# Performance work log

Hardware: AMD Instinct MI355X
Metric: run time of the kernel (lower is better)

The kernel has to match this reference:

```python
import jax, jax.numpy as jnp
import numpy as np

N_HEAD = 16
N_EMBD = 1024
HEAD_DIM = N_EMBD // N_HEAD  # 64
ROPE_BASE = 10000.0


def _rotary_cos_sin(T, dim, dtype=jnp.float32):
    # matches Rotary: inv_freq over even indices, cos/sin cached in bfloat16
    inv_freq = 1.0 / (ROPE_BASE ** (jnp.arange(0, dim, 2, dtype=jnp.float32) / dim))
    freqs = jnp.arange(T, dtype=jnp.float32)[:, None] * inv_freq[None, :]  # [T, dim/2]
    cos = jnp.cos(freqs).astype(jnp.bfloat16).astype(dtype)
    sin = jnp.sin(freqs).astype(jnp.bfloat16).astype(dtype)
    # shape [1, T, 1, dim/2] to broadcast over (B, T, H, d)
    return cos[None, :, None, :], sin[None, :, None, :]


def _apply_rotary(x, cos, sin):
    d = x.shape[3] // 2
    x1, x2 = x[..., :d], x[..., d:]
    y1 = x1 * cos + x2 * sin
    y2 = -x1 * sin + x2 * cos
    return jnp.concatenate([y1, y2], axis=3).astype(x.dtype)


def setup_inputs() -> dict:
    key = jax.random.key(0)
    ks = jax.random.split(key, 8)
    B, T, C = 2, 2048, N_EMBD
    scale = C ** -0.5  # realistic linear-layer init scale
    x = jax.random.normal(ks[0], (B, T, C), dtype=jnp.float32)
    Wq1 = jax.random.normal(ks[1], (C, C), dtype=jnp.float32) * scale
    Wk1 = jax.random.normal(ks[2], (C, C), dtype=jnp.float32) * scale
    Wq2 = jax.random.normal(ks[3], (C, C), dtype=jnp.float32) * scale
    Wk2 = jax.random.normal(ks[4], (C, C), dtype=jnp.float32) * scale
    Wv = jax.random.normal(ks[5], (C, C), dtype=jnp.float32) * scale
    Wout = jax.random.normal(ks[6], (C, C), dtype=jnp.float32) * scale
    return {"x": x, "Wq1": Wq1, "Wk1": Wk1, "Wq2": Wq2, "Wk2": Wk2, "Wv": Wv, "Wout": Wout}


def reference(x, Wq1, Wk1, Wq2, Wk2, Wv, Wout):
    B, T, C = x.shape
    H, D = N_HEAD, HEAD_DIM

    def proj(W):
        # torch nn.Linear(bias=False): y = x @ W.T
        return (x @ W.T).reshape(B, T, H, D)

    q1, k1 = proj(Wq1), proj(Wk1)
    q2, k2 = proj(Wq2), proj(Wk2)
    v = proj(Wv)

    cos, sin = _rotary_cos_sin(T, D, x.dtype)
    q1, k1 = _apply_rotary(q1, cos, sin), _apply_rotary(k1, cos, sin)
    q2, k2 = _apply_rotary(q2, cos, sin), _apply_rotary(k2, cos, sin)

    # two bilinear score maps, elementwise product, causal mask
    s1 = jnp.einsum('bqhd,bkhd->bhqk', q1, k1)  # [B,H,T,T]
    s2 = jnp.einsum('bqhd,bkhd->bhqk', q2, k2)
    causal = jnp.tril(jnp.ones((T, T), dtype=bool))
    pattern = jnp.where(causal[None, None], (s1 / D) * (s2 / D), 0.0)

    y = jnp.einsum('bhqk,bkhd->bqhd', pattern, v).reshape(B, T, C)
    return y @ Wout.T
```

## Files before the change

### kernel.cpp

```cpp
#include <hip/hip_runtime.h>
#include <hip/hip_bf16.h>
#include <math.h>

typedef __bf16 bf16;
typedef __bf16 bf16x8 __attribute__((ext_vector_type(8)));
typedef float  f32x4  __attribute__((ext_vector_type(4)));

#define NB    2
#define NT    2048
#define NH    16
#define ND    64
#define NC    1024
#define NBT   4096
#define NQT   32

#define AS1C(p) ((const __attribute__((address_space(1))) void*)(p))
#define AS3(p)  ((__attribute__((address_space(3))) void*)(p))

#define MFMA(a,b,c) __builtin_amdgcn_mfma_f32_16x16x32_bf16(a, b, c, 0, 0, 0)

__global__ void cast_kernel(const float* __restrict__ src, bf16* __restrict__ dst, int n)
{
    int i = (blockIdx.x * blockDim.x + threadIdx.x) * 4;
    if (i + 3 < n) {
        float4 v = *reinterpret_cast<const float4*>(src + i);
        dst[i+0] = (bf16)v.x;
        dst[i+1] = (bf16)v.y;
        dst[i+2] = (bf16)v.z;
        dst[i+3] = (bf16)v.w;
    }
}

struct WPtrs { const float* p[6]; };
__global__ void cast6_kernel(WPtrs w, bf16* __restrict__ dst)
{
    const int mat = blockIdx.x >> 10;
    const int off = ((blockIdx.x & 1023) * 256 + threadIdx.x) * 4;
    float4 v = *reinterpret_cast<const float4*>(w.p[mat] + off);
    bf16* d = dst + (size_t)mat * NC * NC + off;
    d[0] = (bf16)v.x; d[1] = (bf16)v.y; d[2] = (bf16)v.z; d[3] = (bf16)v.w;
}

__global__ void rope_table_kernel(float2* __restrict__ tbl)
{
    int i = blockIdx.x * 256 + threadIdx.x;
    int t = i >> 5, j = i & 31;
    float invf = 1.0f / powf(10000.0f, (float)j * (1.0f/32.0f));
    float fr = (float)t * invf;
    float2 cs;
    cs.x = (float)(bf16)cosf(fr);
    cs.y = (float)(bf16)sinf(fr);
    tbl[i] = cs;
}

__global__ __launch_bounds__(512, 1)
void gemm_proj(const bf16* __restrict__ A, const bf16* __restrict__ Bw,
               bf16* __restrict__ qkv, const float2* __restrict__ tbl)
{
    __shared__ bf16 smem[2*32768];

    const int tid  = threadIdx.x;
    const int lane = tid & 63;
    const int w    = tid >> 6;
    const int wr   = w >> 2;
    const int wc   = w & 3;

    const int id  = blockIdx.x;
    const int swz = (id & 7) * 40 + (id >> 3);
    const int by  = swz / 20, bx = swz % 20;
    const int row0 = by * 256, col0 = bx * 256;

    const int lo  = lane & 15;
    const int hi  = lane >> 4;

    const int srow = tid >> 3;
    const int ssw  = ((tid & 7) ^ (srow & 7)) * 8;

    f32x4 acc[8][4] = {};

    auto stage = [&](int buf, int kt) {
        char* As = (char*)smem + buf*65536;
        char* Bs = As + 32768;
        #pragma unroll
        for (int i = 0; i < 4; ++i) {
            const unsigned loff = (unsigned)(i*8192 + w*1024);
            __builtin_amdgcn_global_load_lds(
                AS1C(A + (size_t)(row0 + i*64 + srow) * NC + kt + ssw),
                AS3(As + loff), 16, 0, 0);
            __builtin_amdgcn_global_load_lds(
                AS1C(Bw + (size_t)(col0 + i*64 + srow) * NC + kt + ssw),
                AS3(Bs + loff), 16, 0, 0);
        }
    };

    stage(0, 0);
    asm volatile("s_waitcnt vmcnt(0)" ::: "memory");
    __syncthreads();

    for (int kt = 0; kt < 16; ++kt) {
        const int cur = kt & 1;
        if (kt < 15) stage(cur ^ 1, (kt + 1) * 64);

        const char* As = (const char*)smem + cur*65536;
        const char* Bs = As + 32768;

        __builtin_amdgcn_s_setprio(1);
        #pragma unroll
        for (int ks = 0; ks < 2; ++ks) {
            bf16x8 af[8], bfr[4];
            #pragma unroll
            for (int m = 0; m < 8; ++m) {
                const int ar = wr*128 + m*16 + lo;
                af[m] = *reinterpret_cast<const bf16x8*>(
                    As + ar*128 + (((ks*4 + hi) ^ (lo & 7)) * 16));
            }
            #pragma unroll
            for (int n = 0; n < 4; ++n) {
                const int br = wc*64 + n*16 + lo;
                bfr[n] = *reinterpret_cast<const bf16x8*>(
                    Bs + br*128 + (((ks*4 + hi) ^ (lo & 7)) * 16));
            }
            #pragma unroll
            for (int m = 0; m < 8; ++m)
                #pragma unroll
                for (int n = 0; n < 4; ++n)
                    acc[m][n] = MFMA(af[m], bfr[n], acc[m][n]);
        }
        __builtin_amdgcn_s_setprio(0);

        asm volatile("s_waitcnt vmcnt(0)" ::: "memory");
        __syncthreads();
    }

    bf16* Ct = smem;
    const int p  = col0 >> 10;
    const int h0 = (col0 >> 6) & (NH-1);
    const int rb = hi * 4;

    if (p < 4) {
        const float qsc = (p == 0 || p == 2) ? 0.015625f : 1.0f;
        #pragma unroll
        for (int m = 0; m < 8; ++m)
            #pragma unroll
            for (int r = 0; r < 4; ++r) {
                const int rl = wr*128 + m*16 + rb + r;
                const int t  = (row0 + rl) & (NT-1);
                const unsigned key = ((unsigned)(rl >> 2) & 3) << 5;
                #pragma unroll
                for (int n = 0; n < 2; ++n) {
                    const int j = n*16 + lo;
                    float2 cs = tbl[t*32 + j];
                    float a1 = acc[m][n][r];
                    float a2 = acc[m][n+2][r];
                    const int c1 = wc*64 + j;
                    const int c2 = c1 + 32;
                    *(bf16*)((char*)Ct + (unsigned)(rl*512 + (((unsigned)c1*2) ^ key)))
                        = (bf16)((a1*cs.x + a2*cs.y) * qsc);
                    *(bf16*)((char*)Ct + (unsigned)(rl*512 + (((unsigned)c2*2) ^ key)))
                        = (bf16)((a2*cs.x - a1*cs.y) * qsc);
                }
            }
        __syncthreads();
        #pragma unroll
        for (int it = 0; it < 16; ++it) {
            const int chunk = it*512 + tid;
            const int rl = chunk >> 5;
            const int cc = chunk & 31;
            const unsigned key = ((unsigned)(rl >> 2) & 3) << 5;
            bf16x8 val = *reinterpret_cast<const bf16x8*>(
                (const char*)Ct + (unsigned)(rl*512 + (((unsigned)cc*16) ^ key)));
            const int rowg = row0 + rl;
            const int b = rowg >> 11;
            const int t = rowg & (NT-1);
            const int hh = h0 + (cc >> 3);
            const int d  = (cc & 7) * 8;
            *reinterpret_cast<bf16x8*>(
                qkv + ((((size_t)p*NB + b)*NH + hh)*NT + t)*ND + d) = val;
        }
    } else {
        #pragma unroll
        for (int m = 0; m < 8; ++m)
            #pragma unroll
            for (int r = 0; r < 4; ++r) {
                const int rl = wr*128 + m*16 + rb + r;
                #pragma unroll
                for (int n = 0; n < 4; ++n) {
                    const int c = wc*64 + n*16 + lo;
                    *(bf16*)((char*)Ct + (unsigned)(c*512 + (((unsigned)rl*2) ^ ((c&7)<<4))))
                        = (bf16)acc[m][n][r];
                }
            }
        __syncthreads();
        const int b  = row0 >> 11;
        const int t0 = row0 & (NT-1);
        #pragma unroll
        for (int it = 0; it < 16; ++it) {
            const int chunk = it*512 + tid;
            const int c   = chunk >> 5;
            const int tcc = chunk & 31;
            bf16x8 val = *reinterpret_cast<const bf16x8*>(
                (const char*)Ct + (unsigned)(c*512 + (((unsigned)tcc*16) ^ ((c&7)<<4))));
            const int hh = h0 + (c >> 6);
            const int d  = c & 63;
            *reinterpret_cast<bf16x8*>(
                qkv + (((size_t)4*NB + b)*NH + hh)*(size_t)NT*ND
                    + (size_t)d*NT + t0 + tcc*8) = val;
        }
    }
}

__global__ __launch_bounds__(256)
void gemm_out(const bf16* __restrict__ A, const bf16* __restrict__ Bw,
              float* __restrict__ Cp, int M, int N, int K)
{
    __shared__ bf16 smem[128*128];
    bf16* As = smem;
    bf16* Bs = smem + 128*64;

    const int tid  = threadIdx.x;
    const int lane = tid & 63;
    const int w    = tid >> 6;
    const int wr   = w >> 1;
    const int wc   = w & 1;
    const int row0 = blockIdx.y * 128;
    const int col0 = blockIdx.x * 128;

    const int lo   = lane & 15;
    const int hi8  = (lane >> 4) * 8;
    const int srow = w * 8 + (lane >> 3);
    const int scol = (lane & 7) * 8;

    f32x4 acc[4][4] = {};

    for (int kt = 0; kt < K; kt += 64) {
        #pragma unroll
        for (int i = 0; i < 4; ++i) {
            const unsigned loff = (unsigned)(i * 4096 + w * 1024);
            __builtin_amdgcn_global_load_lds(
                AS1C(A + (size_t)(row0 + i*32 + srow) * K + kt + scol),
                AS3((char*)As + loff), 16, 0, 0);
            __builtin_amdgcn_global_load_lds(
                AS1C(Bw + (size_t)(col0 + i*32 + srow) * K + kt + scol),
                AS3((char*)Bs + loff), 16, 0, 0);
        }
        __syncthreads();
        #pragma unroll
        for (int ks = 0; ks < 2; ++ks) {
            bf16x8 af[4], bfr[4];
            #pragma unroll
            for (int m = 0; m < 4; ++m)
                af[m] = *reinterpret_cast<const bf16x8*>(&As[(wr*64 + m*16 + lo)*64 + ks*32 + hi8]);
            #pragma unroll
            for (int n = 0; n < 4; ++n)
                bfr[n] = *reinterpret_cast<const bf16x8*>(&Bs[(wc*64 + n*16 + lo)*64 + ks*32 + hi8]);
            #pragma unroll
            for (int m = 0; m < 4; ++m)
                #pragma unroll
                for (int n = 0; n < 4; ++n)
                    acc[m][n] = MFMA(af[m], bfr[n], acc[m][n]);
        }
        __syncthreads();
    }

    const int rb = (lane >> 4) * 4;
    #pragma unroll
    for (int m = 0; m < 4; ++m)
        #pragma unroll
        for (int n = 0; n < 4; ++n)
            #pragma unroll
            for (int r = 0; r < 4; ++r) {
                int row = row0 + wr*64 + m*16 + rb + r;
                int col = col0 + wc*64 + n*16 + lo;
                Cp[(size_t)row * N + col] = acc[m][n][r];
            }
}

__global__ __launch_bounds__(256, 2)
void attn_kernel(const bf16* __restrict__ qkv, bf16* __restrict__ Y)
{
    __shared__ bf16 K1s[2*4096];
    __shared__ bf16 K2s[2*4096];
    __shared__ bf16 Vts[2*4096];
    __shared__ bf16 Pa [4][1024];
    __shared__ bf16 Pb [4][1024];

    const int tid  = threadIdx.x;
    const int lane = tid & 63;
    const int w    = tid >> 6;

    const int lin  = blockIdx.x;
    const int xcd  = lin & 7;
    const int slot = lin >> 3;
    const int pair = xcd * 4 + (slot >> 4);
    const int qa   = slot & 15;
    const int h    = pair >> 1;
    const int b    = pair & 1;
    const int qb   = NQT - 1 - qa;

    const size_t plane = (size_t)NB * NH * NT * ND;
    const size_t bh    = ((size_t)b * NH + h) * (size_t)NT * ND;
    const bf16* Q1 = qkv + 0*plane + bh;
    const bf16* K1 = qkv + 1*plane + bh;
    const bf16* Q2 = qkv + 2*plane + bh;
    const bf16* K2 = qkv + 3*plane + bh;
    const bf16* V  = qkv + 4*plane + bh;

    const int lo  = lane & 15;
    const int hi  = lane >> 4;
    const int hi8 = hi * 8;

    bf16x8 q1fa[2], q2fa[2], q1fb[2], q2fb[2];
    #pragma unroll
    for (int dd = 0; dd < 2; ++dd) {
        const size_t ra  = (size_t)(qa*64 + w*16 + lo) * ND + dd*32 + hi8;
        const size_t rbq = (size_t)(qb*64 + w*16 + lo) * ND + dd*32 + hi8;
        q1fa[dd] = *reinterpret_cast<const bf16x8*>(Q1 + ra);
        q2fa[dd] = *reinterpret_cast<const bf16x8*>(Q2 + ra);
        q1fb[dd] = *reinterpret_cast<const bf16x8*>(Q1 + rbq);
        q2fb[dd] = *reinterpret_cast<const bf16x8*>(Q2 + rbq);
    }

    f32x4 yacca[4] = {}, yaccb[4] = {};

    const int srow = tid >> 3;
    const int ssw  = ((tid & 7) ^ (srow & 7)) * 8;

    auto stageK = [&](int buf, int k0) {
        #pragma unroll
        for (int i = 0; i < 2; ++i) {
            const unsigned loff = (unsigned)(buf*8192 + i*4096 + w*1024);
            __builtin_amdgcn_global_load_lds(
                AS1C(K1 + (size_t)(k0 + i*32 + srow) * ND + ssw),
                AS3((char*)K1s + loff), 16, 0, 0);
            __builtin_amdgcn_global_load_lds(
                AS1C(K2 + (size_t)(k0 + i*32 + srow) * ND + ssw),
                AS3((char*)K2s + loff), 16, 0, 0);
        }
    };
    auto stageVT = [&](int buf, int k0) {
        #pragma unroll
        for (int i = 0; i < 2; ++i) {
            const int inst = w*2 + i;
            const int d    = inst*8 + (lane >> 3);
            const int sc   = ((lane & 7) ^ ((lane >> 3) & 7)) * 8;
            __builtin_amdgcn_global_load_lds(
                AS1C(V + (size_t)d * NT + k0 + sc),
                AS3((char*)Vts + (unsigned)(buf*8192 + inst*1024)), 16, 0, 0);
        }
    };

    stageK(0, 0);
    stageVT(0, 0);
    asm volatile("s_waitcnt vmcnt(0)" ::: "memory");
    __syncthreads();

    for (int kt = 0; kt <= qb; ++kt) {
        const int  cur = kt & 1;
        const bool pre = (kt < qb);
        const bool doA = (kt <= qa);
        const int  k0  = kt * 64;

        if (pre) { stageK(cur^1, k0 + 64); stageVT(cur^1, k0 + 64); }

        const bf16* K1b = K1s + cur*4096;
        const bf16* K2b = K2s + cur*4096;

        f32x4 s1a[4] = {}, s2a[4] = {}, s1b[4] = {}, s2b[4] = {};
        __builtin_amdgcn_s_setprio(1);
        #pragma unroll
        for (int dd = 0; dd < 2; ++dd)
            #pragma unroll
            for (int sub = 0; sub < 4; ++sub) {
                const unsigned kb = (unsigned)((sub*16 + lo)*128 + (((dd*4 + hi) ^ (lo & 7)) * 16));
                bf16x8 k1f = *reinterpret_cast<const bf16x8*>((const char*)K1b + kb);
                bf16x8 k2f = *reinterpret_cast<const bf16x8*>((const char*)K2b + kb);
                s1b[sub] = MFMA(q1fb[dd], k1f, s1b[sub]);
                s2b[sub] = MFMA(q2fb[dd], k2f, s2b[sub]);
                if (doA) {
                    s1a[sub] = MFMA(q1fa[dd], k1f, s1a[sub]);
                    s2a[sub] = MFMA(q2fa[dd], k2f, s2a[sub]);
                }
            }
        __builtin_amdgcn_s_setprio(0);

        #define COMBINE(S1, S2, PB, DIAG)                                              \
            _Pragma("unroll")                                                          \
            for (int sub = 0; sub < 4; ++sub)                                          \
                _Pragma("unroll")                                                      \
                for (int r = 0; r < 4; ++r) {                                          \
                    const int row = hi*4 + r;                                          \
                    const int col = sub*16 + lo;                                       \
                    const unsigned byte = (unsigned)(row*128 + (((col>>3) ^ (row&7))*16) + (col&7)*2); \
                    float pv = S1[sub][r] * S2[sub][r];                                \
                    if (DIAG && col > w*16 + row) pv = 0.0f;                           \
                    *(bf16*)((char*)PB + byte) = (bf16)pv;                             \
                }
        if (kt == qb) { COMBINE(s1b, s2b, Pb[w], true) } else { COMBINE(s1b, s2b, Pb[w], false) }
        if (doA) {
            if (kt == qa) { COMBINE(s1a, s2a, Pa[w], true) } else { COMBINE(s1a, s2a, Pa[w], false) }
        }
        #undef COMBINE

        asm volatile("s_waitcnt lgkmcnt(0)" ::: "memory");
        __builtin_amdgcn_sched_barrier(0);

        __builtin_amdgcn_s_setprio(1);
        #pragma unroll
        for (int ks = 0; ks < 2; ++ks) {
            const unsigned pby = (unsigned)(lo*128 + (((ks*4 + hi) ^ (lo & 7)) * 16));
            bf16x8 pfb = *reinterpret_cast<const bf16x8*>((const char*)Pb[w] + pby);
            bf16x8 pfa = {};
            if (doA) pfa = *reinterpret_cast<const bf16x8*>((const char*)Pa[w] + pby);
            #pragma unroll
            for (int n = 0; n < 4; ++n) {
                const unsigned vby = (unsigned)(cur*8192 + (n*16 + lo)*128 + (((ks*4 + hi) ^ (lo & 7)) * 16));
                bf16x8 vf = *reinterpret_cast<const bf16x8*>((const char*)Vts + vby);
                yaccb[n] = MFMA(pfb, vf, yaccb[n]);
                if (doA) yacca[n] = MFMA(pfa, vf, yacca[n]);
            }
        }
        __builtin_amdgcn_s_setprio(0);

        asm volatile("s_waitcnt vmcnt(0)" ::: "memory");
        __syncthreads();
    }

    auto writeOut = [&](int q0, const f32x4* ya, bf16* Pbuf) {
        #pragma unroll
        for (int n = 0; n < 4; ++n)
            #pragma unroll
            for (int r = 0; r < 4; ++r) {
                const int row = hi*4 + r;
                const int col = n*16 + lo;
                const unsigned byte = (unsigned)(row*128 + (((col>>3) ^ (row&7))*16) + (col&7)*2);
                *(bf16*)((char*)Pbuf + byte) = (bf16)ya[n][r];
            }
        asm volatile("s_waitcnt lgkmcnt(0)" ::: "memory");
        __builtin_amdgcn_sched_barrier(0);
        #pragma unroll
        for (int pass = 0; pass < 2; ++pass) {
            const int idx = pass*64 + lane;
            const int row = idx >> 3;
            const int cc  = idx & 7;
            bf16x8 val = *reinterpret_cast<const bf16x8*>(
                (const char*)Pbuf + row*128 + ((cc ^ (row&7))*16));
            const int t = q0 + w*16 + row;
            const int c = h*ND + cc*8;
            *reinterpret_cast<bf16x8*>(Y + ((size_t)b*NT + t)*NC + c) = val;
        }
    };
    writeOut(qa*64, yacca, Pa[w]);
    writeOut(qb*64, yaccb, Pb[w]);
}

extern "C" void kernel_launch(void* const* d_in, const int* in_sizes, int n_in,
                              void* d_out, int out_size, void* d_ws, size_t ws_size,
                              hipStream_t stream)
{
    const float* x = (const float*)d_in[0];

    char* ws = (char*)d_ws;
    bf16*   Xbf   = (bf16*)ws;
    bf16*   Wcat  = (bf16*)(ws + (size_t)NBT*NC*2);
    bf16*   QKV   = (bf16*)(ws + (size_t)NBT*NC*2 + (size_t)6*NC*NC*2);
    bf16*   Ybf   = (bf16*)((char*)QKV + (size_t)5*NBT*NC*2);
    float2* tbl   = (float2*)((char*)Ybf + (size_t)NBT*NC*2);
    bf16*   Woutb = Wcat + (size_t)5*NC*NC;

    cast_kernel<<<dim3(NBT*NC/1024), 256, 0, stream>>>(x, Xbf, NBT*NC);
    WPtrs wp;
    wp.p[0] = (const float*)d_in[1]; wp.p[1] = (const float*)d_in[2];
    wp.p[2] = (const float*)d_in[3]; wp.p[3] = (const float*)d_in[4];
    wp.p[4] = (const float*)d_in[5]; wp.p[5] = (const float*)d_in[6];
    cast6_kernel<<<dim3(6*1024), 256, 0, stream>>>(wp, Wcat);
    rope_table_kernel<<<dim3(NT*32/256), 256, 0, stream>>>(tbl);

    gemm_proj<<<dim3(320), 512, 0, stream>>>(Xbf, Wcat, QKV, tbl);
    attn_kernel<<<dim3(512), 256, 0, stream>>>(QKV, Ybf);
    gemm_out<<<dim3(NC/128, NBT/128), 256, 0, stream>>>(Ybf, Woutb, (float*)d_out, NBT, NC, NC);
}
```

Before: 169.8 us.

## Split paired query tiles into separate blocks and stage V through registers

Each attention block now handles a single 64-row query tile rather than a balanced pair (qa, 31-qa). The grid doubles to 1024 blocks, with heavy and light tiles interleaved across slots. V is loaded into registers and written into a single LDS buffer after the compute, which removes one V buffer and one P buffer. The smaller LDS footprint lets the launch bound rise to 3 blocks per CU. The cost is that each K/V tile load now feeds half as many MFMAs, so load reuse drops, and the extra barriers plus uneven per-block work can hurt load balance.

Result: slower. 178.4 us (+5.1%).

```diff
diff --git a/kernel.cpp b/kernel.cpp
--- a/kernel.cpp
+++ b/kernel.cpp
@@ -275,14 +275,13 @@
             }
 }
 
-__global__ __launch_bounds__(256, 2)
+__global__ __launch_bounds__(256, 3)
 void attn_kernel(const bf16* __restrict__ qkv, bf16* __restrict__ Y)
 {
     __shared__ bf16 K1s[2*4096];
     __shared__ bf16 K2s[2*4096];
-    __shared__ bf16 Vts[2*4096];
-    __shared__ bf16 Pa [4][1024];
-    __shared__ bf16 Pb [4][1024];
+    __shared__ bf16 Vts[4096];
+    __shared__ bf16 Pl [4][1024];
 
     const int tid  = threadIdx.x;
     const int lane = tid & 63;
@@ -291,11 +290,12 @@
     const int lin  = blockIdx.x;
     const int xcd  = lin & 7;
     const int slot = lin >> 3;
-    const int pair = xcd * 4 + (slot >> 4);
-    const int qa   = slot & 15;
+    const int pair = xcd * 4 + (slot >> 5);
+    const int s    = slot & 31;
+    const int q    = (s & 1) ? (NQT - 1 - (s >> 1)) : (s >> 1);
     const int h    = pair >> 1;
     const int b    = pair & 1;
-    const int qb   = NQT - 1 - qa;
+    const int q0   = q * 64;
 
     const size_t plane = (size_t)NB * NH * NT * ND;
     const size_t bh    = ((size_t)b * NH + h) * (size_t)NT * ND;
@@ -309,18 +309,15 @@
     const int hi  = lane >> 4;
     const int hi8 = hi * 8;
 
-    bf16x8 q1fa[2], q2fa[2], q1fb[2], q2fb[2];
+    bf16x8 q1f[2], q2f[2];
     #pragma unroll
     for (int dd = 0; dd < 2; ++dd) {
-        const size_t ra  = (size_t)(qa*64 + w*16 + lo) * ND + dd*32 + hi8;
-        const size_t rbq = (size_t)(qb*64 + w*16 + lo) * ND + dd*32 + hi8;
-        q1fa[dd] = *reinterpret_cast<const bf16x8*>(Q1 + ra);
-        q2fa[dd] = *reinterpret_cast<const bf16x8*>(Q2 + ra);
-        q1fb[dd] = *reinterpret_cast<const bf16x8*>(Q1 + rbq);
-        q2fb[dd] = *reinterpret_cast<const bf16x8*>(Q2 + rbq);
-    }
-
-    f32x4 yacca[4] = {}, yaccb[4] = {};
+        const size_t ra = (size_t)(q0 + w*16 + lo) * ND + dd*32 + hi8;
+        q1f[dd] = *reinterpret_cast<const bf16x8*>(Q1 + ra);
+        q2f[dd] = *reinterpret_cast<const bf16x8*>(Q2 + ra);
+    }
+
+    f32x4 yacc[4] = {};
 
     const int srow = tid >> 3;
     const int ssw  = ((tid & 7) ^ (srow & 7)) * 8;
@@ -337,35 +334,42 @@
                 AS3((char*)K2s + loff), 16, 0, 0);
         }
     };
-    auto stageVT = [&](int buf, int k0) {
-        #pragma unroll
-        for (int i = 0; i < 2; ++i) {
-            const int inst = w*2 + i;
-            const int d    = inst*8 + (lane >> 3);
-            const int sc   = ((lane & 7) ^ ((lane >> 3) & 7)) * 8;
-            __builtin_amdgcn_global_load_lds(
-                AS1C(V + (size_t)d * NT + k0 + sc),
-                AS3((char*)Vts + (unsigned)(buf*8192 + inst*1024)), 16, 0, 0);
-        }
+
+    const int vd_  = tid >> 3;
+    const int vtc  = tid & 7;
+    auto loadV = [&](int k0, bf16x8* vr) {
+        #pragma unroll
+        for (int j = 0; j < 2; ++j)
+            vr[j] = *reinterpret_cast<const bf16x8*>(
+                V + (size_t)(j*32 + vd_) * NT + k0 + vtc*8);
     };
-
+    auto writeV = [&](const bf16x8* vr) {
+        #pragma unroll
+        for (int j = 0; j < 2; ++j) {
+            const int d = j*32 + vd_;
+            *reinterpret_cast<bf16x8*>(
+                (char*)Vts + (unsigned)(d*128 + ((vtc ^ (d&7))*16))) = vr[j];
+        }
+    };
+
+    bf16x8 vr[2];
     stageK(0, 0);
-    stageVT(0, 0);
+    loadV(0, vr);
+    writeV(vr);
     asm volatile("s_waitcnt vmcnt(0)" ::: "memory");
     __syncthreads();
 
-    for (int kt = 0; kt <= qb; ++kt) {
+    for (int kt = 0; kt <= q; ++kt) {
         const int  cur = kt & 1;
-        const bool pre = (kt < qb);
-        const bool doA = (kt <= qa);
+        const bool pre = (kt < q);
         const int  k0  = kt * 64;
 
-        if (pre) { stageK(cur^1, k0 + 64); stageVT(cur^1, k0 + 64); }
+        if (pre) { stageK(cur^1, k0 + 64); loadV(k0 + 64, vr); }
 
         const bf16* K1b = K1s + cur*4096;
         const bf16* K2b = K2s + cur*4096;
 
-        f32x4 s1a[4] = {}, s2a[4] = {}, s1b[4] = {}, s2b[4] = {};
+        f32x4 s1[4] = {}, s2[4] = {};
         __builtin_amdgcn_s_setprio(1);
         #pragma unroll
         for (int dd = 0; dd < 2; ++dd)
@@ -374,16 +378,12 @@
                 const unsigned kb = (unsigned)((sub*16 + lo)*128 + (((dd*4 + hi) ^ (lo & 7)) * 16));
                 bf16x8 k1f = *reinterpret_cast<const bf16x8*>((const char*)K1b + kb);
                 bf16x8 k2f = *reinterpret_cast<const bf16x8*>((const char*)K2b + kb);
-                s1b[sub] = MFMA(q1fb[dd], k1f, s1b[sub]);
-                s2b[sub] = MFMA(q2fb[dd], k2f, s2b[sub]);
-                if (doA) {
-                    s1a[sub] = MFMA(q1fa[dd], k1f, s1a[sub]);
-                    s2a[sub] = MFMA(q2fa[dd], k2f, s2a[sub]);
-                }
+                s1[sub] = MFMA(q1f[dd], k1f, s1[sub]);
+                s2[sub] = MFMA(q2f[dd], k2f, s2[sub]);
             }
         __builtin_amdgcn_s_setprio(0);
 
-        #define COMBINE(S1, S2, PB, DIAG)                                              \
+        #define COMBINE(DIAG)                                                          \
             _Pragma("unroll")                                                          \
             for (int sub = 0; sub < 4; ++sub)                                          \
                 _Pragma("unroll")                                                      \
@@ -391,14 +391,11 @@
                     const int row = hi*4 + r;                                          \
                     const int col = sub*16 + lo;                                       \
                     const unsigned byte = (unsigned)(row*128 + (((col>>3) ^ (row&7))*16) + (col&7)*2); \
-                    float pv = S1[sub][r] * S2[sub][r];                                \
+                    float pv = s1[sub][r] * s2[sub][r];                                \
                     if (DIAG && col > w*16 + row) pv = 0.0f;                           \
-                    *(bf16*)((char*)PB + byte) = (bf16)pv;                             \
+                    *(bf16*)((char*)Pl[w] + byte) = (bf16)pv;                          \
                 }
-        if (kt == qb) { COMBINE(s1b, s2b, Pb[w], true) } else { COMBINE(s1b, s2b, Pb[w], false) }
-        if (doA) {
-            if (kt == qa) { COMBINE(s1a, s2a, Pa[w], true) } else { COMBINE(s1a, s2a, Pa[w], false) }
-        }
+        if (kt == q) { COMBINE(true) } else { COMBINE(false) }
         #undef COMBINE
 
         asm volatile("s_waitcnt lgkmcnt(0)" ::: "memory");
@@ -408,49 +405,46 @@
         #pragma unroll
         for (int ks = 0; ks < 2; ++ks) {
             const unsigned pby = (unsigned)(lo*128 + (((ks*4 + hi) ^ (lo & 7)) * 16));
-            bf16x8 pfb = *reinterpret_cast<const bf16x8*>((const char*)Pb[w] + pby);
-            bf16x8 pfa = {};
-            if (doA) pfa = *reinterpret_cast<const bf16x8*>((const char*)Pa[w] + pby);
+            bf16x8 pf = *reinterpret_cast<const bf16x8*>((const char*)Pl[w] + pby);
             #pragma unroll
             for (int n = 0; n < 4; ++n) {
-                const unsigned vby = (unsigned)(cur*8192 + (n*16 + lo)*128 + (((ks*4 + hi) ^ (lo & 7)) * 16));
+                const unsigned vby = (unsigned)((n*16 + lo)*128 + (((ks*4 + hi) ^ (lo & 7)) * 16));
                 bf16x8 vf = *reinterpret_cast<const bf16x8*>((const char*)Vts + vby);
-                yaccb[n] = MFMA(pfb, vf, yaccb[n]);
-                if (doA) yacca[n] = MFMA(pfa, vf, yacca[n]);
+                yacc[n] = MFMA(pf, vf, yacc[n]);
             }
         }
         __builtin_amdgcn_s_setprio(0);
 
-        asm volatile("s_waitcnt vmcnt(0)" ::: "memory");
-        __syncthreads();
-    }
-
-    auto writeOut = [&](int q0, const f32x4* ya, bf16* Pbuf) {
-        #pragma unroll
-        for (int n = 0; n < 4; ++n)
-            #pragma unroll
-            for (int r = 0; r < 4; ++r) {
-                const int row = hi*4 + r;
-                const int col = n*16 + lo;
-                const unsigned byte = (unsigned)(row*128 + (((col>>3) ^ (row&7))*16) + (col&7)*2);
-                *(bf16*)((char*)Pbuf + byte) = (bf16)ya[n][r];
-            }
-        asm volatile("s_waitcnt lgkmcnt(0)" ::: "memory");
-        __builtin_amdgcn_sched_barrier(0);
-        #pragma unroll
-        for (int pass = 0; pass < 2; ++pass) {
-            const int idx = pass*64 + lane;
-            const int row = idx >> 3;
-            const int cc  = idx & 7;
-            bf16x8 val = *reinterpret_cast<const bf16x8*>(
-                (const char*)Pbuf + row*128 + ((cc ^ (row&7))*16));
-            const int t = q0 + w*16 + row;
-            const int c = h*ND + cc*8;
-            *reinterpret_cast<bf16x8*>(Y + ((size_t)b*NT + t)*NC + c) = val;
-        }
-    };
-    writeOut(qa*64, yacca, Pa[w]);
-    writeOut(qb*64, yaccb, Pb[w]);
+        if (pre) {
+            __syncthreads();
+            writeV(vr);
+            asm volatile("s_waitcnt vmcnt(0)" ::: "memory");
+            __syncthreads();
+        }
+    }
+
+    #pragma unroll
+    for (int n = 0; n < 4; ++n)
+        #pragma unroll
+        for (int r = 0; r < 4; ++r) {
+            const int row = hi*4 + r;
+            const int col = n*16 + lo;
+            const unsigned byte = (unsigned)(row*128 + (((col>>3) ^ (row&7))*16) + (col&7)*2);
+            *(bf16*)((char*)Pl[w] + byte) = (bf16)yacc[n][r];
+        }
+    asm volatile("s_waitcnt lgkmcnt(0)" ::: "memory");
+    __builtin_amdgcn_sched_barrier(0);
+    #pragma unroll
+    for (int pass = 0; pass < 2; ++pass) {
+        const int idx = pass*64 + lane;
+        const int row = idx >> 3;
+        const int cc  = idx & 7;
+        bf16x8 val = *reinterpret_cast<const bf16x8*>(
+            (const char*)Pl[w] + row*128 + ((cc ^ (row&7))*16));
+        const int t = q0 + w*16 + row;
+        const int c = h*ND + cc*8;
+        *reinterpret_cast<bf16x8*>(Y + ((size_t)b*NT + t)*NC + c) = val;
+    }
 }
 
 extern "C" void kernel_launch(void* const* d_in, const int* in_sizes, int n_in,
@@ -476,6 +470,6 @@
     rope_table_kernel<<<dim3(NT*32/256), 256, 0, stream>>>(tbl);
 
     gemm_proj<<<dim3(320), 512, 0, stream>>>(Xbf, Wcat, QKV, tbl);
-    attn_kernel<<<dim3(512), 256, 0, stream>>>(QKV, Ybf);
+    attn_kernel<<<dim3(1024), 256, 0, stream>>>(QKV, Ybf);
     gemm_out<<<dim3(NC/128, NBT/128), 256, 0, stream>>>(Ybf, Woutb, (float*)d_out, NBT, NC, NC);
 }
```

## Double-buffer and XOR-swizzle LDS tiles in output projection GEMM

Applied to the files above, without the earlier changes.

Rewrites the output-projection GEMM so the next K tile is prefetched into a second LDS buffer while MFMAs run on the current one. It also applies an XOR swizzle to LDS row chunks to avoid bank conflicts on fragment reads, raises wave priority during the MFMA phase, and hardcodes the dimensions. The aim is to hide global load latency and cut LDS conflicts. In exchange, LDS use doubles to 64KB per block, which may lower occupancy.

Result: faster. 161.6 us (-4.8%).

```diff
diff --git a/kernel.cpp b/kernel.cpp
--- a/kernel.cpp
+++ b/kernel.cpp
@@ -211,11 +211,9 @@
 
 __global__ __launch_bounds__(256)
 void gemm_out(const bf16* __restrict__ A, const bf16* __restrict__ Bw,
-              float* __restrict__ Cp, int M, int N, int K)
-{
-    __shared__ bf16 smem[128*128];
-    bf16* As = smem;
-    bf16* Bs = smem + 128*64;
+              float* __restrict__ Cp)
+{
+    __shared__ bf16 smem[2*16384];
 
     const int tid  = threadIdx.x;
     const int lane = tid & 63;
@@ -225,44 +223,69 @@
     const int row0 = blockIdx.y * 128;
     const int col0 = blockIdx.x * 128;
 
-    const int lo   = lane & 15;
-    const int hi8  = (lane >> 4) * 8;
-    const int srow = w * 8 + (lane >> 3);
-    const int scol = (lane & 7) * 8;
+    const int lo  = lane & 15;
+    const int hi  = lane >> 4;
+
+    const int srow = tid >> 3;
+    const int ssw  = ((tid & 7) ^ (srow & 7)) * 8;
 
     f32x4 acc[4][4] = {};
 
-    for (int kt = 0; kt < K; kt += 64) {
+    auto stage = [&](int buf, int kt) {
+        char* As = (char*)smem + buf*32768;
+        char* Bs = As + 16384;
         #pragma unroll
         for (int i = 0; i < 4; ++i) {
-            const unsigned loff = (unsigned)(i * 4096 + w * 1024);
-            __builtin_amdgcn_global_load_lds(
-                AS1C(A + (size_t)(row0 + i*32 + srow) * K + kt + scol),
-                AS3((char*)As + loff), 16, 0, 0);
-            __builtin_amdgcn_global_load_lds(
-                AS1C(Bw + (size_t)(col0 + i*32 + srow) * K + kt + scol),
-                AS3((char*)Bs + loff), 16, 0, 0);
-        }
-        __syncthreads();
+            const unsigned loff = (unsigned)(i*4096 + w*1024);
+            __builtin_amdgcn_global_load_lds(
+                AS1C(A + (size_t)(row0 + i*32 + srow) * NC + kt + ssw),
+                AS3(As + loff), 16, 0, 0);
+            __builtin_amdgcn_global_load_lds(
+                AS1C(Bw + (size_t)(col0 + i*32 + srow) * NC + kt + ssw),
+                AS3(Bs + loff), 16, 0, 0);
+        }
+    };
+
+    stage(0, 0);
+    asm volatile("s_waitcnt vmcnt(0)" ::: "memory");
+    __syncthreads();
+
+    for (int kt = 0; kt < 16; ++kt) {
+        const int cur = kt & 1;
+        if (kt < 15) stage(cur ^ 1, (kt + 1) * 64);
+
+        const char* As = (const char*)smem + cur*32768;
+        const char* Bs = As + 16384;
+
+        __builtin_amdgcn_s_setprio(1);
         #pragma unroll
         for (int ks = 0; ks < 2; ++ks) {
             bf16x8 af[4], bfr[4];
             #pragma unroll
-            for (int m = 0; m < 4; ++m)
-                af[m] = *reinterpret_cast<const bf16x8*>(&As[(wr*64 + m*16 + lo)*64 + ks*32 + hi8]);
-            #pragma unroll
-            for (int n = 0; n < 4; ++n)
-                bfr[n] = *reinterpret_cast<const bf16x8*>(&Bs[(wc*64 + n*16 + lo)*64 + ks*32 + hi8]);
+            for (int m = 0; m < 4; ++m) {
+                const int ar = wr*64 + m*16 + lo;
+                af[m] = *reinterpret_cast<const bf16x8*>(
+                    As + ar*128 + (((ks*4 + hi) ^ (lo & 7)) * 16));
+            }
+            #pragma unroll
+            for (int n = 0; n < 4; ++n) {
+                const int br = wc*64 + n*16 + lo;
+                bfr[n] = *reinterpret_cast<const bf16x8*>(
+                    Bs + br*128 + (((ks*4 + hi) ^ (lo & 7)) * 16));
+            }
             #pragma unroll
             for (int m = 0; m < 4; ++m)
                 #pragma unroll
                 for (int n = 0; n < 4; ++n)
                     acc[m][n] = MFMA(af[m], bfr[n], acc[m][n]);
         }
+        __builtin_amdgcn_s_setprio(0);
+
+        asm volatile("s_waitcnt vmcnt(0)" ::: "memory");
         __syncthreads();
     }
 
-    const int rb = (lane >> 4) * 4;
+    const int rb = hi * 4;
     #pragma unroll
     for (int m = 0; m < 4; ++m)
         #pragma unroll
@@ -271,7 +294,7 @@
             for (int r = 0; r < 4; ++r) {
                 int row = row0 + wr*64 + m*16 + rb + r;
                 int col = col0 + wc*64 + n*16 + lo;
-                Cp[(size_t)row * N + col] = acc[m][n][r];
+                Cp[(size_t)row * NC + col] = acc[m][n][r];
             }
 }
 
@@ -477,5 +500,5 @@
 
     gemm_proj<<<dim3(320), 512, 0, stream>>>(Xbf, Wcat, QKV, tbl);
     attn_kernel<<<dim3(512), 256, 0, stream>>>(QKV, Ybf);
-    gemm_out<<<dim3(NC/128, NBT/128), 256, 0, stream>>>(Ybf, Woutb, (float*)d_out, NBT, NC, NC);
-}
+    gemm_out<<<dim3(NC/128, NBT/128), 256, 0, stream>>>(Ybf, Woutb, (float*)d_out);
+}
```
